# Optimization experiments

Measured on AMD Instinct MI355X. Metric: run time of the kernel, lower is better.

Reference implementation:

```python
import jax, jax.numpy as jnp
import numpy as np

NUM_HEADS = 16
HEAD_DIM = 80
DIM = NUM_HEADS * HEAD_DIM
SEQ = 2048
SCALE = HEAD_DIM ** -0.5


def rotate_half(x):
    x1, x2 = jnp.split(x, 2, axis=-1)
    return jnp.concatenate((-x2, x1), axis=-1)


def setup_inputs() -> dict:
    key = jax.random.key(0)
    ks = jax.random.split(key, 8)
    hidden_states = jax.random.normal(ks[0], (SEQ, DIM), dtype=jnp.float32)
    cu_seqlens = jnp.array([0, SEQ], dtype=jnp.int32)  # unused by the math
    # rotary embeddings for head_dim
    inv_freq = 1.0 / (10000.0 ** (jnp.arange(0, HEAD_DIM // 2, dtype=jnp.float32) / (HEAD_DIM // 2)))
    freqs = jnp.outer(jnp.arange(SEQ, dtype=jnp.float32), inv_freq)  # [S, hd/2]
    emb = jnp.concatenate((freqs, freqs), axis=-1)  # [S, hd]
    cos = jnp.cos(emb)
    sin = jnp.sin(emb)
    w_qkv = jax.random.normal(ks[1], (3 * DIM, DIM), dtype=jnp.float32) * (DIM ** -0.5)
    b_qkv = jax.random.normal(ks[2], (3 * DIM,), dtype=jnp.float32) * 0.02
    w_proj = jax.random.normal(ks[3], (DIM, DIM), dtype=jnp.float32) * (DIM ** -0.5)
    b_proj = jax.random.normal(ks[4], (DIM,), dtype=jnp.float32) * 0.02
    return {"hidden_states": hidden_states, "cu_seqlens": cu_seqlens, "cos": cos,
            "sin": sin, "w_qkv": w_qkv, "b_qkv": b_qkv, "w_proj": w_proj, "b_proj": b_proj}


def reference(hidden_states, cu_seqlens, cos, sin, w_qkv, b_qkv, w_proj, b_proj):
    S = hidden_states.shape[0]
    qkv = hidden_states @ w_qkv.T + b_qkv  # [S, 3*D]
    qkv = qkv.reshape(S, 3, NUM_HEADS, HEAD_DIM)
    q, k, v = qkv[:, 0], qkv[:, 1], qkv[:, 2]  # each [S, H, hd]
    c = cos[:, None, :]  # [S, 1, hd]
    s = sin[:, None, :]
    q = q * c + rotate_half(q) * s
    k = k * c + rotate_half(k) * s
    # SDPA, non-causal: [H, S, S]
    scores = jnp.einsum('shd,thd->hst', q, k) * SCALE
    attn = jax.nn.softmax(scores, axis=-1)
    out = jnp.einsum('hst,thd->shd', attn, v).reshape(S, DIM)
    return out @ w_proj.T + b_proj
```

## Files before the change

kernel.cpp:

```cpp
#include <hip/hip_runtime.h>


#define SEQLEN   2048
#define DIMM     1280
#define NHEADS   16
#define HD       80
#define HDP      96
#define QKV_N    3840
#define NSPLIT   2
#define KVSPAN   (SEQLEN / NSPLIT)
#define QSCALE_LOG2E 0.16130083587064776f

#define KSTRIDE  104
#define VSTRIDE  72
#define PSTRIDE  72

#define EXP2F(x) __builtin_amdgcn_exp2f(x)

#define GLD16(gptr, lptr)                                                      \
    __builtin_amdgcn_global_load_lds(                                          \
        (const __attribute__((address_space(1))) void*)(gptr),                 \
        (__attribute__((address_space(3))) void*)(lptr), 16, 0, 0)

typedef float f32x4 __attribute__((ext_vector_type(4)));
typedef _Float16 half8 __attribute__((ext_vector_type(8)));
typedef _Float16 half4 __attribute__((ext_vector_type(4)));

static __device__ __forceinline__ f32x4 mfma_16x16x32(half8 a, half8 b, f32x4 c) {
    return __builtin_amdgcn_mfma_f32_16x16x32_f16(a, b, c, 0, 0, 0);
}

__global__ void cast_f32_f16(const float* __restrict__ src,
                             _Float16* __restrict__ dst, int n4) {
    int i = blockIdx.x * blockDim.x + threadIdx.x;
    if (i < n4) {
        const float4 v = ((const float4*)src)[i];
        half4 h;
        h.x = (_Float16)v.x; h.y = (_Float16)v.y;
        h.z = (_Float16)v.z; h.w = (_Float16)v.w;
        ((half4*)dst)[i] = h;
    }
}

template<bool OUT_F16>
__global__ __launch_bounds__(256, 2)
void gemm_bt(const _Float16* __restrict__ A, const _Float16* __restrict__ B,
             const float* __restrict__ bias, void* __restrict__ Cout,
             int M, int N, int K) {
    __shared__ __align__(16) _Float16 As[128 * 32];
    __shared__ __align__(16) _Float16 Bs[128 * 32];
    const int tid  = threadIdx.x;
    const int lane = tid & 63;
    const int wave = tid >> 6;
    const int l15  = lane & 15;
    const int quad = lane >> 4;
    const int wm   = wave & 1;
    const int wn   = wave >> 1;
    const long bm = blockIdx.x, bn = blockIdx.y;

    const _Float16* Ag = A + bm * 128 * (long)K;
    const _Float16* Bg = B + bn * 128 * (long)K;

    const int srow = lane >> 2;
    const int scol = (lane & 3) * 8;
    f32x4 acc[4][4] = {};

    for (int k0 = 0; k0 < K; k0 += 32) {
        __syncthreads();
#pragma unroll
        for (int cc = 0; cc < 2; cc++) {
            const int c = wave + cc * 4;
            const long row = 16 * c + srow;
            GLD16(Ag + row * K + k0 + scol, As + 512 * c + lane * 8);
            GLD16(Bg + row * K + k0 + scol, Bs + 512 * c + lane * 8);
        }
        __syncthreads();
        half8 af[4], bf[4];
#pragma unroll
        for (int t = 0; t < 4; t++) {
            af[t] = *(const half8*)&As[(wm * 64 + t * 16 + l15) * 32 + quad * 8];
            bf[t] = *(const half8*)&Bs[(wn * 64 + t * 16 + l15) * 32 + quad * 8];
        }
#pragma unroll
        for (int mt = 0; mt < 4; mt++)
#pragma unroll
            for (int nt = 0; nt < 4; nt++)
                acc[mt][nt] = mfma_16x16x32(af[mt], bf[nt], acc[mt][nt]);
    }

    float bv[4];
#pragma unroll
    for (int nt = 0; nt < 4; nt++)
        bv[nt] = bias[bn * 128 + wn * 64 + nt * 16 + l15];

#pragma unroll
    for (int mt = 0; mt < 4; mt++) {
#pragma unroll
        for (int r = 0; r < 4; r++) {
            const long row = bm * 128 + wm * 64 + mt * 16 + quad * 4 + r;
#pragma unroll
            for (int nt = 0; nt < 4; nt++) {
                const long col = bn * 128 + wn * 64 + nt * 16 + l15;
                const float v = acc[mt][nt][r] + bv[nt];
                if (OUT_F16) ((_Float16*)Cout)[row * (long)N + col] = (_Float16)v;
                else         ((float*)Cout)[row * (long)N + col] = v;
            }
        }
    }
}

__global__ void rope_repack(const _Float16* __restrict__ qkv,
                            const float* __restrict__ cosb,
                            const float* __restrict__ sinb,
                            _Float16* __restrict__ Qh,
                            _Float16* __restrict__ Kh,
                            _Float16* __restrict__ Vh) {
    const int s = blockIdx.x;
    const int tid = threadIdx.x;
    const _Float16* row = qkv + (long)s * QKV_N;

    for (int i = tid; i < NHEADS * 40; i += 256) {
        const int h = i / 40, d = i - h * 40;
        const float c  = cosb[s * HD + d];
        const float sn = sinb[s * HD + d];
        const long o = ((long)h * SEQLEN + s) * HDP;
        const float q0 = (float)row[h * HD + d];
        const float q1 = (float)row[h * HD + d + 40];
        Qh[o + d]      = (_Float16)((q0 * c - q1 * sn) * QSCALE_LOG2E);
        Qh[o + d + 40] = (_Float16)((q1 * c + q0 * sn) * QSCALE_LOG2E);
        const float k0 = (float)row[DIMM + h * HD + d];
        const float k1 = (float)row[DIMM + h * HD + d + 40];
        Kh[o + d]      = (_Float16)(k0 * c - k1 * sn);
        Kh[o + d + 40] = (_Float16)(k1 * c + k0 * sn);
    }
    for (int i = tid; i < NHEADS * HD; i += 256) {
        const int h = i / HD, d = i - h * HD;
        Vh[((long)h * SEQLEN + s) * HDP + d] = row[2 * DIMM + i];
    }
    for (int i = tid; i < NHEADS * 16; i += 256) {
        const int h = i >> 4, d = HD + (i & 15);
        const long o = ((long)h * SEQLEN + s) * HDP + d;
        Qh[o] = (_Float16)0.f; Kh[o] = (_Float16)0.f;
    }
}

__global__ __launch_bounds__(256)
void v_transpose(const _Float16* __restrict__ Vh, _Float16* __restrict__ Vt) {
    const int s0 = blockIdx.x * 64;
    const int h  = blockIdx.y;
    __shared__ __align__(16) _Float16 Ts[64 * 88];
    const int tid = threadIdx.x;
    for (int i = tid; i < 640; i += 256) {
        const int r = i / 10, c = (i - r * 10) * 8;
        *(half8*)&Ts[r * 88 + c] =
            *(const half8*)&Vh[((long)h * SEQLEN + s0 + r) * HDP + c];
    }
    __syncthreads();
    for (int i = tid; i < 640; i += 256) {
        const int d = i >> 3, sc = (i & 7) * 8;
        half8 v;
#pragma unroll
        for (int j = 0; j < 8; j++) v[j] = Ts[(sc + j) * 88 + d];
        *(half8*)&Vt[((long)h * HD + d) * SEQLEN + s0 + sc] = v;
    }
}

__global__ __launch_bounds__(256, 4)
void attn_kernel(const _Float16* __restrict__ Qh, const _Float16* __restrict__ Kh,
                 const _Float16* __restrict__ Vt, _Float16* __restrict__ Ohat,
                 float* __restrict__ Lpart) {
    const int s0 = blockIdx.x * 64;
    const int h  = blockIdx.y;
    const int z  = blockIdx.z;
    __shared__ __align__(16) _Float16 Ks[64 * KSTRIDE];
    __shared__ __align__(16) _Float16 Vts[HD * VSTRIDE];
    __shared__ __align__(16) _Float16 Ps[4][16 * PSTRIDE];

    const int tid  = threadIdx.x;
    const int lane = tid & 63;
    const int wave = tid >> 6;
    const int l15  = lane & 15;
    const int quad = lane >> 4;

    const _Float16* Qg = Qh + ((long)h * SEQLEN + s0 + wave * 16 + l15) * HDP;
    half8 qf[3];
#pragma unroll
    for (int kk = 0; kk < 3; kk++)
        qf[kk] = *(const half8*)&Qg[kk * 32 + quad * 8];

    f32x4 oacc[5] = {};
    float l_r[4] = {0.f, 0.f, 0.f, 0.f};

    for (int t0 = z * KVSPAN; t0 < (z + 1) * KVSPAN; t0 += 64) {
        __syncthreads();
        const _Float16* Kg = Kh + ((long)h * SEQLEN + t0) * HDP;
        for (int i = tid; i < 768; i += 256) {
            const int r = i / 12, c = (i - r * 12) * 8;
            *(half8*)&Ks[r * KSTRIDE + c] = *(const half8*)&Kg[(long)r * HDP + c];
        }
        const _Float16* Vtg = Vt + (long)h * HD * SEQLEN + t0;
        for (int i = tid; i < 640; i += 256) {
            const int d = i >> 3, c = (i & 7) * 8;
            *(half8*)&Vts[d * VSTRIDE + c] = *(const half8*)&Vtg[(long)d * SEQLEN + c];
        }
        __syncthreads();

        f32x4 sa[4] = {};
#pragma unroll
        for (int kk = 0; kk < 3; kk++)
#pragma unroll
            for (int ct = 0; ct < 4; ct++) {
                half8 b = *(const half8*)&Ks[(ct * 16 + l15) * KSTRIDE + kk * 32 + quad * 8];
                sa[ct] = mfma_16x16x32(qf[kk], b, sa[ct]);
            }

        float p[4][4];
#pragma unroll
        for (int ct = 0; ct < 4; ct++)
#pragma unroll
            for (int r = 0; r < 4; r++) {
                p[ct][r] = EXP2F(sa[ct][r]);
                l_r[r] += p[ct][r];
                Ps[wave][(quad * 4 + r) * PSTRIDE + ct * 16 + l15] = (_Float16)p[ct][r];
            }
        asm volatile("s_waitcnt lgkmcnt(0)" ::: "memory");
        half8 pf0 = *(const half8*)&Ps[wave][l15 * PSTRIDE + quad * 8];
        half8 pf1 = *(const half8*)&Ps[wave][l15 * PSTRIDE + 32 + quad * 8];
#pragma unroll
        for (int nt = 0; nt < 5; nt++) {
            half8 v0 = *(const half8*)&Vts[(nt * 16 + l15) * VSTRIDE + quad * 8];
            half8 v1 = *(const half8*)&Vts[(nt * 16 + l15) * VSTRIDE + 32 + quad * 8];
            oacc[nt] = mfma_16x16x32(pf0, v0, oacc[nt]);
            oacc[nt] = mfma_16x16x32(pf1, v1, oacc[nt]);
        }
    }

#pragma unroll
    for (int off = 1; off < 16; off <<= 1)
#pragma unroll
        for (int r = 0; r < 4; r++)
            l_r[r] += __shfl_xor(l_r[r], off);

    float inv[4];
#pragma unroll
    for (int r = 0; r < 4; r++) inv[r] = 1.0f / l_r[r];

    const long base = ((long)z * NHEADS + h) * SEQLEN;
#pragma unroll
    for (int nt = 0; nt < 5; nt++)
#pragma unroll
        for (int r = 0; r < 4; r++) {
            const long row = s0 + wave * 16 + quad * 4 + r;
            Ohat[(base + row) * HD + nt * 16 + l15] = (_Float16)(oacc[nt][r] * inv[r]);
        }
    if (l15 == 0)
#pragma unroll
        for (int r = 0; r < 4; r++)
            Lpart[base + s0 + wave * 16 + quad * 4 + r] = l_r[r];
}

__global__ __launch_bounds__(256)
void attn_combine(const _Float16* __restrict__ Ohat, const float* __restrict__ Lp,
                  _Float16* __restrict__ attnb) {
    const int i = blockIdx.x * 256 + threadIdx.x;
    if (i >= SEQLEN * DIMM / 4) return;
    const int flat = i * 4;
    const int s = flat / DIMM;
    const int rem = flat - s * DIMM;
    const int h = rem / HD;
    const int d = rem - h * HD;
    const float l0 = Lp[h * SEQLEN + s];
    const float l1 = Lp[(NHEADS + h) * SEQLEN + s];
    const float invl = 1.0f / (l0 + l1);
    const float w0 = l0 * invl, w1 = l1 * invl;
    const half4 o0 = *(const half4*)&Ohat[((long)h * SEQLEN + s) * HD + d];
    const half4 o1 = *(const half4*)&Ohat[((long)(NHEADS + h) * SEQLEN + s) * HD + d];
    half4 o;
#pragma unroll
    for (int j = 0; j < 4; j++)
        o[j] = (_Float16)((float)o0[j] * w0 + (float)o1[j] * w1);
    *(half4*)&attnb[(long)s * DIMM + rem] = o;
}

extern "C" void kernel_launch(void* const* d_in, const int* in_sizes, int n_in,
                              void* d_out, int out_size, void* d_ws, size_t ws_size,
                              hipStream_t stream) {
    const float* hs     = (const float*)d_in[0];
    const float* cosb   = (const float*)d_in[2];
    const float* sinb   = (const float*)d_in[3];
    const float* w_qkv  = (const float*)d_in[4];
    const float* b_qkv  = (const float*)d_in[5];
    const float* w_proj = (const float*)d_in[6];
    const float* b_proj = (const float*)d_in[7];
    float* out = (float*)d_out;

    _Float16* hsb    = (_Float16*)d_ws;
    _Float16* wqkvb  = hsb    + (long)SEQLEN * DIMM;
    _Float16* wprojb = wqkvb  + (long)QKV_N * DIMM;
    _Float16* qkv    = wprojb + (long)DIMM * DIMM;
    _Float16* Qh     = qkv    + (long)SEQLEN * QKV_N;
    _Float16* Kh     = Qh     + (long)NHEADS * SEQLEN * HDP;
    _Float16* Vh     = Kh     + (long)NHEADS * SEQLEN * HDP;
    _Float16* Vtb    = Vh     + (long)NHEADS * SEQLEN * HDP;
    _Float16* attnb  = Vtb    + (long)NHEADS * HD * SEQLEN;

    _Float16* OhatB  = (_Float16*)d_ws;
    float*    LpartB = (float*)(OhatB + (long)NSPLIT * NHEADS * SEQLEN * HD);

    {
        int n4 = SEQLEN * DIMM / 4;
        cast_f32_f16<<<(n4 + 255) / 256, 256, 0, stream>>>(hs, hsb, n4);
        n4 = QKV_N * DIMM / 4;
        cast_f32_f16<<<(n4 + 255) / 256, 256, 0, stream>>>(w_qkv, wqkvb, n4);
        n4 = DIMM * DIMM / 4;
        cast_f32_f16<<<(n4 + 255) / 256, 256, 0, stream>>>(w_proj, wprojb, n4);
    }

    gemm_bt<true><<<dim3(SEQLEN / 128, QKV_N / 128), 256, 0, stream>>>(
        hsb, wqkvb, b_qkv, qkv, SEQLEN, QKV_N, DIMM);

    rope_repack<<<SEQLEN, 256, 0, stream>>>(qkv, cosb, sinb, Qh, Kh, Vh);

    v_transpose<<<dim3(SEQLEN / 64, NHEADS), 256, 0, stream>>>(Vh, Vtb);

    attn_kernel<<<dim3(SEQLEN / 64, NHEADS, NSPLIT), 256, 0, stream>>>(
        Qh, Kh, Vtb, OhatB, LpartB);

    attn_combine<<<(SEQLEN * DIMM / 4 + 255) / 256, 256, 0, stream>>>(
        OhatB, LpartB, attnb);

    gemm_bt<false><<<dim3(SEQLEN / 128, DIMM / 128), 256, 0, stream>>>(
        attnb, wprojb, b_proj, out, SEQLEN, DIMM, DIMM);
}
```

Baseline: 232.0 us.

## Shrink attention blocks, load V directly to registers, split-K output projection

The attention kernel now uses 128-thread blocks covering 32 queries, and each wave reads its V fragments straight from global memory into registers instead of staging V in shared memory. This drops the V shared-memory buffer and its sync, and doubles the block count. The output projection GEMM is replaced by a split-K version with two K halves that accumulates into a zeroed output with float atomics, which doubles its grid to fill more CUs. The cost is an extra memset, atomic traffic, and redundant global V reads across waves that now have to be served from cache.

```diff
diff --git a/kernel.cpp b/kernel.cpp
--- a/kernel.cpp
+++ b/kernel.cpp
@@ -12,7 +12,6 @@
 #define QSCALE_LOG2E 0.16130083587064776f
 
 #define KSTRIDE  104
-#define VSTRIDE  72
 #define PSTRIDE  72
 
 #define EXP2F(x) __builtin_amdgcn_exp2f(x)
@@ -109,6 +108,72 @@
     }
 }
 
+__global__ __launch_bounds__(256, 2)
+void gemm_bt_sk(const _Float16* __restrict__ A, const _Float16* __restrict__ B,
+                const float* __restrict__ bias, float* __restrict__ Cout,
+                int M, int N, int K) {
+    __shared__ __align__(16) _Float16 As[128 * 32];
+    __shared__ __align__(16) _Float16 Bs[128 * 32];
+    const int tid  = threadIdx.x;
+    const int lane = tid & 63;
+    const int wave = tid >> 6;
+    const int l15  = lane & 15;
+    const int quad = lane >> 4;
+    const int wm   = wave & 1;
+    const int wn   = wave >> 1;
+    const long bm = blockIdx.x, bn = blockIdx.y;
+    const int  z  = blockIdx.z;
+    const int  kHalf = K / 2;
+
+    const _Float16* Ag = A + bm * 128 * (long)K;
+    const _Float16* Bg = B + bn * 128 * (long)K;
+
+    const int srow = lane >> 2;
+    const int scol = (lane & 3) * 8;
+    f32x4 acc[4][4] = {};
+
+    for (int k0 = z * kHalf; k0 < (z + 1) * kHalf; k0 += 32) {
+        __syncthreads();
+#pragma unroll
+        for (int cc = 0; cc < 2; cc++) {
+            const int c = wave + cc * 4;
+            const long row = 16 * c + srow;
+            GLD16(Ag + row * K + k0 + scol, As + 512 * c + lane * 8);
+            GLD16(Bg + row * K + k0 + scol, Bs + 512 * c + lane * 8);
+        }
+        __syncthreads();
+        half8 af[4], bf[4];
+#pragma unroll
+        for (int t = 0; t < 4; t++) {
+            af[t] = *(const half8*)&As[(wm * 64 + t * 16 + l15) * 32 + quad * 8];
+            bf[t] = *(const half8*)&Bs[(wn * 64 + t * 16 + l15) * 32 + quad * 8];
+        }
+#pragma unroll
+        for (int mt = 0; mt < 4; mt++)
+#pragma unroll
+            for (int nt = 0; nt < 4; nt++)
+                acc[mt][nt] = mfma_16x16x32(af[mt], bf[nt], acc[mt][nt]);
+    }
+
+    float bv[4];
+#pragma unroll
+    for (int nt = 0; nt < 4; nt++)
+        bv[nt] = (z == 0) ? bias[bn * 128 + wn * 64 + nt * 16 + l15] : 0.f;
+
+#pragma unroll
+    for (int mt = 0; mt < 4; mt++) {
+#pragma unroll
+        for (int r = 0; r < 4; r++) {
+            const long row = bm * 128 + wm * 64 + mt * 16 + quad * 4 + r;
+#pragma unroll
+            for (int nt = 0; nt < 4; nt++) {
+                const long col = bn * 128 + wn * 64 + nt * 16 + l15;
+                unsafeAtomicAdd(&Cout[row * (long)N + col], acc[mt][nt][r] + bv[nt]);
+            }
+        }
+    }
+}
+
 __global__ void rope_repack(const _Float16* __restrict__ qkv,
                             const float* __restrict__ cosb,
                             const float* __restrict__ sinb,
@@ -165,16 +230,15 @@
     }
 }
 
-__global__ __launch_bounds__(256, 4)
+__global__ __launch_bounds__(128)
 void attn_kernel(const _Float16* __restrict__ Qh, const _Float16* __restrict__ Kh,
                  const _Float16* __restrict__ Vt, _Float16* __restrict__ Ohat,
                  float* __restrict__ Lpart) {
-    const int s0 = blockIdx.x * 64;
+    const int s0 = blockIdx.x * 32;
     const int h  = blockIdx.y;
     const int z  = blockIdx.z;
     __shared__ __align__(16) _Float16 Ks[64 * KSTRIDE];
-    __shared__ __align__(16) _Float16 Vts[HD * VSTRIDE];
-    __shared__ __align__(16) _Float16 Ps[4][16 * PSTRIDE];
+    __shared__ __align__(16) _Float16 Ps[2][16 * PSTRIDE];
 
     const int tid  = threadIdx.x;
     const int lane = tid & 63;
@@ -188,22 +252,27 @@
     for (int kk = 0; kk < 3; kk++)
         qf[kk] = *(const half8*)&Qg[kk * 32 + quad * 8];
 
+    const _Float16* VtH = Vt + (long)h * HD * SEQLEN;
+
     f32x4 oacc[5] = {};
     float l_r[4] = {0.f, 0.f, 0.f, 0.f};
 
     for (int t0 = z * KVSPAN; t0 < (z + 1) * KVSPAN; t0 += 64) {
         __syncthreads();
         const _Float16* Kg = Kh + ((long)h * SEQLEN + t0) * HDP;
-        for (int i = tid; i < 768; i += 256) {
+        for (int i = tid; i < 768; i += 128) {
             const int r = i / 12, c = (i - r * 12) * 8;
             *(half8*)&Ks[r * KSTRIDE + c] = *(const half8*)&Kg[(long)r * HDP + c];
         }
-        const _Float16* Vtg = Vt + (long)h * HD * SEQLEN + t0;
-        for (int i = tid; i < 640; i += 256) {
-            const int d = i >> 3, c = (i & 7) * 8;
-            *(half8*)&Vts[d * VSTRIDE + c] = *(const half8*)&Vtg[(long)d * SEQLEN + c];
-        }
-        __syncthreads();
+        __syncthreads();
+
+        half8 v0[5], v1[5];
+#pragma unroll
+        for (int nt = 0; nt < 5; nt++) {
+            const _Float16* vr = VtH + (long)(nt * 16 + l15) * SEQLEN + t0;
+            v0[nt] = *(const half8*)&vr[quad * 8];
+            v1[nt] = *(const half8*)&vr[32 + quad * 8];
+        }
 
         f32x4 sa[4] = {};
 #pragma unroll
@@ -228,10 +297,8 @@
         half8 pf1 = *(const half8*)&Ps[wave][l15 * PSTRIDE + 32 + quad * 8];
 #pragma unroll
         for (int nt = 0; nt < 5; nt++) {
-            half8 v0 = *(const half8*)&Vts[(nt * 16 + l15) * VSTRIDE + quad * 8];
-            half8 v1 = *(const half8*)&Vts[(nt * 16 + l15) * VSTRIDE + 32 + quad * 8];
-            oacc[nt] = mfma_16x16x32(pf0, v0, oacc[nt]);
-            oacc[nt] = mfma_16x16x32(pf1, v1, oacc[nt]);
+            oacc[nt] = mfma_16x16x32(pf0, v0[nt], oacc[nt]);
+            oacc[nt] = mfma_16x16x32(pf1, v1[nt], oacc[nt]);
         }
     }
 
@@ -323,12 +390,13 @@
 
     v_transpose<<<dim3(SEQLEN / 64, NHEADS), 256, 0, stream>>>(Vh, Vtb);
 
-    attn_kernel<<<dim3(SEQLEN / 64, NHEADS, NSPLIT), 256, 0, stream>>>(
+    attn_kernel<<<dim3(SEQLEN / 32, NHEADS, NSPLIT), 128, 0, stream>>>(
         Qh, Kh, Vtb, OhatB, LpartB);
 
     attn_combine<<<(SEQLEN * DIMM / 4 + 255) / 256, 256, 0, stream>>>(
         OhatB, LpartB, attnb);
 
-    gemm_bt<false><<<dim3(SEQLEN / 128, DIMM / 128), 256, 0, stream>>>(
+    hipMemsetAsync(out, 0, (size_t)SEQLEN * DIMM * sizeof(float), stream);
+    gemm_bt_sk<<<dim3(SEQLEN / 128, DIMM / 128, 2), 256, 0, stream>>>(
         attnb, wprojb, b_proj, out, SEQLEN, DIMM, DIMM);
 }
```

After: 275.4 us. +18.7%, slower.
